# Kernel optimization log

Hardware: AMD Instinct MI355X
Metric: run time of the kernel (lower is better)

The kernel has to match this reference:

```python
import jax, jax.numpy as jnp
import numpy as np

N_HEADS = 8
N_POINTS = 4
SPATIAL = np.array([[64, 64], [32, 32], [16, 16], [8, 8]], dtype=np.int32)


def setup_inputs() -> dict:
    key = jax.random.key(0)
    ks = jax.random.split(key, 12)
    d = 256
    H, L, P, N = N_HEADS, SPATIAL.shape[0], N_POINTS, 8
    lens = SPATIAL[:, 0] * SPATIAL[:, 1]
    Lin = int(lens.sum())
    Lq = Lin
    query = jax.random.normal(ks[0], (N, Lq, d), jnp.float32)
    reference_points = jax.random.uniform(ks[1], (N, Lq, L, 2), jnp.float32)
    input_flatten = jax.random.normal(ks[2], (N, Lin, d), jnp.float32)
    input_spatial_shapes = jnp.asarray(SPATIAL)
    starts = np.concatenate([[0], np.cumsum(lens)[:-1]]).astype(np.int32)
    input_level_start_index = jnp.asarray(starts)
    s = 1.0 / np.sqrt(d)
    W_off = jax.random.normal(ks[3], (H * L * P * 2, d), jnp.float32) * 0.01
    b_off = jax.random.normal(ks[4], (H * L * P * 2,), jnp.float32) * 0.5
    W_attn = jax.random.normal(ks[5], (H * L * P, d), jnp.float32) * 0.02
    b_attn = jnp.zeros((H * L * P,), jnp.float32)
    W_val = jax.random.normal(ks[6], (d, d), jnp.float32) * s
    b_val = jnp.zeros((d,), jnp.float32)
    W_out = jax.random.normal(ks[7], (d, d), jnp.float32) * s
    b_out = jnp.zeros((d,), jnp.float32)
    return {
        'query': query, 'reference_points': reference_points,
        'input_flatten': input_flatten,
        'input_spatial_shapes': input_spatial_shapes,
        'input_level_start_index': input_level_start_index,
        'W_off': W_off, 'b_off': b_off, 'W_attn': W_attn, 'b_attn': b_attn,
        'W_val': W_val, 'b_val': b_val, 'W_out': W_out, 'b_out': b_out,
    }


def _bilinear(img, Hl, Wl, x, y):
    # img: [B, Ch, Hl*Wl]; x, y: [B, Q, P] pixel coords (align_corners=False)
    # zero padding mode: out-of-range corners contribute 0
    x0 = jnp.floor(x)
    y0 = jnp.floor(y)
    wx = x - x0
    wy = y - y0

    def gather(xi, yi):
        valid = (xi >= 0) & (xi <= Wl - 1) & (yi >= 0) & (yi <= Hl - 1)
        ii = jnp.clip(xi, 0, Wl - 1).astype(jnp.int32)
        jj = jnp.clip(yi, 0, Hl - 1).astype(jnp.int32)
        idx = jj * Wl + ii  # [B, Q, P]
        B, Q, P = idx.shape
        v = jnp.take_along_axis(img, idx.reshape(B, 1, Q * P), axis=2)
        v = v.reshape(B, img.shape[1], Q, P)
        return v * valid[:, None].astype(img.dtype)

    return (gather(x0, y0) * ((1 - wx) * (1 - wy))[:, None]
            + gather(x0 + 1, y0) * (wx * (1 - wy))[:, None]
            + gather(x0, y0 + 1) * ((1 - wx) * wy)[:, None]
            + gather(x0 + 1, y0 + 1) * (wx * wy)[:, None])


def reference(query, reference_points, input_flatten, input_spatial_shapes,
              input_level_start_index, W_off, b_off, W_attn, b_attn,
              W_val, b_val, W_out, b_out):
    shapes = np.asarray(input_spatial_shapes)  # static structural metadata
    N, Lq, d = query.shape
    Lin = input_flatten.shape[1]
    L = shapes.shape[0]
    H, P = N_HEADS, N_POINTS
    Ch = d // H

    value = input_flatten @ W_val.T + b_val                       # [N, Lin, d]
    value = value.reshape(N, Lin, H, Ch).transpose(0, 2, 3, 1)    # [N, H, Ch, Lin]
    value = value.reshape(N * H, Ch, Lin)

    off = (query @ W_off.T + b_off).reshape(N, Lq, H, L, P, 2)
    attn = (query @ W_attn.T + b_attn).reshape(N, Lq, H, L * P)
    attn = jax.nn.softmax(attn, axis=-1).reshape(N, Lq, H, L, P)

    # normalizer is (W, H) per level
    norm = jnp.asarray(np.stack([shapes[:, 1], shapes[:, 0]], -1), query.dtype)
    loc = reference_points[:, :, None, :, None, :] + off / norm[None, None, None, :, None, :]

    attn_p = attn.transpose(0, 2, 1, 3, 4).reshape(N * H, Lq, L, P)
    starts = np.concatenate([[0], np.cumsum(shapes[:, 0] * shapes[:, 1])])

    out = jnp.zeros((N * H, Ch, Lq), query.dtype)
    for l in range(L):
        Hl, Wl = int(shapes[l, 0]), int(shapes[l, 1])
        v_l = value[:, :, starts[l]:starts[l + 1]]                # [B, Ch, Hl*Wl]
        g = loc[:, :, :, l].transpose(0, 2, 1, 3, 4).reshape(N * H, Lq, P, 2)
        # grid_sample align_corners=False with grid=2*loc-1 -> pixel = loc*W - 0.5
        x = g[..., 0] * Wl - 0.5
        y = g[..., 1] * Hl - 0.5
        samp = _bilinear(v_l, Hl, Wl, x, y)                       # [B, Ch, Lq, P]
        out = out + jnp.einsum('bcqp,bqp->bcq', samp, attn_p[:, :, l])

    out = out.reshape(N, H, Ch, Lq).transpose(0, 3, 1, 2).reshape(N, Lq, d)
    return out @ W_out.T + b_out
```

## Files before the change

kernel.cpp:

```cpp
#include <hip/hip_runtime.h>
#include <hip/hip_bf16.h>

#define NQ   5440
#define NB   8
#define DIM  256
#define NH   8
#define CHN  32
#define NLV  4
#define NPT  4
#define MTOT (NB * NQ)

typedef __attribute__((ext_vector_type(8))) short s16x8;
typedef __attribute__((ext_vector_type(4))) short s16x4;
typedef __attribute__((ext_vector_type(4))) float f32x4;
typedef unsigned short ushort_t;

#define WVAL 0
#define WOFF 65536
#define WATT 131072
#define WOUT 163840
#define WTOT 229376

__device__ __forceinline__ short f2bf(float x) {
    union { __hip_bfloat16 b; short s; } u;
    u.b = __float2bfloat16(x);
    return u.s;
}

__global__ __launch_bounds__(256) void cvt_weights(const float* __restrict__ wv,
                                                   const float* __restrict__ wo,
                                                   const float* __restrict__ wa,
                                                   const float* __restrict__ wu,
                                                   ushort_t* __restrict__ wb) {
    int i = (blockIdx.x * 256 + threadIdx.x) * 4;
    if (i >= WTOT) return;
    const float* src;
    int off;
    if (i < WOFF)       { src = wv; off = WVAL; }
    else if (i < WATT)  { src = wo; off = WOFF; }
    else if (i < WOUT)  { src = wa; off = WATT; }
    else                { src = wu; off = WOUT; }
    f32x4 v = *(const f32x4*)(src + (i - off));
    s16x4 b;
#pragma unroll
    for (int e = 0; e < 4; ++e) b[e] = f2bf(v[e]);
    *(s16x4*)(wb + i) = b;
}

#define LDSK 72

__device__ __forceinline__ s16x8 load8(const float* p) {
    f32x4 a0 = *(const f32x4*)p, a1 = *(const f32x4*)(p + 4);
    s16x8 v;
#pragma unroll
    for (int e = 0; e < 4; ++e) { v[e] = f2bf(a0[e]); v[e + 4] = f2bf(a1[e]); }
    return v;
}
__device__ __forceinline__ s16x8 load8(const ushort_t* p) { return *(const s16x8*)p; }

__device__ __forceinline__ void stC(float* p, float v) { *p = v; }
__device__ __forceinline__ void stC(ushort_t* p, float v) { *(short*)p = f2bf(v); }

template <typename AT, typename CT>
__device__ __forceinline__ void gemm_core(const AT* __restrict__ A,
                                          const ushort_t* __restrict__ Wt,
                                          const float* __restrict__ biasT,
                                          CT* __restrict__ Ct, int ldC, int rowBase) {
    __shared__ short As[128 * LDSK];
    __shared__ short Ws[128 * LDSK];

    const int t = threadIdx.x;
    const int lane = t & 63, wave = t >> 6;
    const int wm = wave >> 1, wn = wave & 1;
    const int lr = lane & 15, quad = lane >> 4;

    f32x4 acc[4][4];
#pragma unroll
    for (int i = 0; i < 4; ++i)
#pragma unroll
        for (int j = 0; j < 4; ++j)
#pragma unroll
            for (int r = 0; r < 4; ++r) acc[i][j][r] = 0.f;

    for (int k0 = 0; k0 < 256; k0 += 64) {
#pragma unroll
        for (int i = 0; i < 4; ++i) {
            int c = t + i * 256;
            int r = c >> 3, kc = (c & 7) * 8;
            *(s16x8*)&As[r * LDSK + kc] = load8(A + (size_t)(rowBase + r) * DIM + k0 + kc);
            *(s16x8*)&Ws[r * LDSK + kc] = load8(Wt + (size_t)r * DIM + k0 + kc);
        }
        __syncthreads();
#pragma unroll
        for (int kk = 0; kk < 64; kk += 32) {
            s16x8 afr[4], wfr[4];
#pragma unroll
            for (int i = 0; i < 4; ++i)
                afr[i] = *(const s16x8*)&As[(wm * 64 + i * 16 + lr) * LDSK + kk + quad * 8];
#pragma unroll
            for (int j = 0; j < 4; ++j)
                wfr[j] = *(const s16x8*)&Ws[(wn * 64 + j * 16 + lr) * LDSK + kk + quad * 8];
#pragma unroll
            for (int i = 0; i < 4; ++i)
#pragma unroll
                for (int j = 0; j < 4; ++j)
                    acc[i][j] = __builtin_amdgcn_mfma_f32_16x16x32_bf16(
                        afr[i], wfr[j], acc[i][j], 0, 0, 0);
        }
        __syncthreads();
    }

    float bj[4];
#pragma unroll
    for (int j = 0; j < 4; ++j) bj[j] = biasT[wn * 64 + j * 16 + lr];
#pragma unroll
    for (int i = 0; i < 4; ++i)
#pragma unroll
        for (int r = 0; r < 4; ++r) {
            int row = rowBase + wm * 64 + i * 16 + quad * 4 + r;
#pragma unroll
            for (int j = 0; j < 4; ++j) {
                int col = wn * 64 + j * 16 + lr;
                stC(&Ct[(size_t)row * ldC + col], acc[i][j][r] + bj[j]);
            }
        }
}

__global__ __launch_bounds__(256) void gemm_val(const float* __restrict__ A,
                                                const ushort_t* __restrict__ wb,
                                                const float* __restrict__ bias,
                                                ushort_t* __restrict__ C) {
    gemm_core<float, ushort_t>(A, wb + WVAL + (size_t)blockIdx.y * 128 * DIM,
                               bias + blockIdx.y * 128, C + blockIdx.y * 128, DIM,
                               blockIdx.x * 128);
}

__global__ __launch_bounds__(256) void gemm_qkv(const float* __restrict__ A,
                                                const ushort_t* __restrict__ wb,
                                                const float* __restrict__ b_off,
                                                const float* __restrict__ b_attn,
                                                float* __restrict__ v_off,
                                                float* __restrict__ v_attn) {
    if (blockIdx.y < 2)
        gemm_core<float, float>(A, wb + WOFF + (size_t)blockIdx.y * 128 * DIM,
                                b_off + blockIdx.y * 128, v_off + blockIdx.y * 128, DIM,
                                blockIdx.x * 128);
    else
        gemm_core<float, float>(A, wb + WATT, b_attn, v_attn, 128, blockIdx.x * 128);
}

__global__ __launch_bounds__(256) void gemm_out(const ushort_t* __restrict__ A,
                                                const ushort_t* __restrict__ wb,
                                                const float* __restrict__ bias,
                                                float* __restrict__ C) {
    gemm_core<ushort_t, float>(A, wb + WOUT + (size_t)blockIdx.y * 128 * DIM,
                               bias + blockIdx.y * 128, C + blockIdx.y * 128, DIM,
                               blockIdx.x * 128);
}

__device__ __forceinline__ f32x4 bf4(uint2 u) {
    f32x4 r;
    r[0] = __uint_as_float(u.x << 16);
    r[1] = __uint_as_float(u.x & 0xffff0000u);
    r[2] = __uint_as_float(u.y << 16);
    r[3] = __uint_as_float(u.y & 0xffff0000u);
    return r;
}

__global__ __launch_bounds__(256) void sample_kernel(
    const float* __restrict__ refp,
    const float* __restrict__ off,
    const float* __restrict__ attn,
    const ushort_t* __restrict__ valb,
    const int* __restrict__ shapes,
    const int* __restrict__ starts,
    ushort_t* __restrict__ sampb)
{
    const int qBase = blockIdx.x * 4;
    const int t = threadIdx.x;

    __shared__ __align__(16) int   sidx[512][4];
    __shared__ __align__(16) float sww[512][4];

#pragma unroll
    for (int it = 0; it < 2; ++it) {
        const int i = t + it * 256;
        const int q4 = i >> 7, hlp = i & 127;
        const int h = hlp >> 4, lp = hlp & 15, l = lp >> 2, p = lp & 3;
        const int q = qBase + q4;
        const int Wl = shapes[2 * l + 1], Hl = shapes[2 * l];
        const float Wf = (float)Wl, Hf = (float)Hl;
        const float rx = refp[((size_t)q * NLV + l) * 2 + 0];
        const float ry = refp[((size_t)q * NLV + l) * 2 + 1];
        const int oidx = ((h * NLV + l) * NPT + p) * 2;
        const float ox = off[(size_t)q * DIM + oidx];
        const float oy = off[(size_t)q * DIM + oidx + 1];
        const float x = (rx + ox / Wf) * Wf - 0.5f;
        const float y = (ry + oy / Hf) * Hf - 0.5f;

        float logit = attn[(size_t)q * 128 + h * 16 + lp];
        float m = logit;
#pragma unroll
        for (int s = 8; s >= 1; s >>= 1) m = fmaxf(m, __shfl_xor(m, s, 16));
        float e = __expf(logit - m);
        float ss = e;
#pragma unroll
        for (int s = 8; s >= 1; s >>= 1) ss += __shfl_xor(ss, s, 16);
        const float aw = e / ss;

        const float xf = floorf(x), yf = floorf(y);
        const int ix = (int)xf, iy = (int)yf;
        const float wx = x - xf, wy = y - yf;
        const int ix1 = ix + 1, iy1 = iy + 1;
        const bool bx0 = (ix >= 0) & (ix < Wl);
        const bool bx1 = (ix1 >= 0) & (ix1 < Wl);
        const bool by0 = (iy >= 0) & (iy < Hl);
        const bool by1 = (iy1 >= 0) & (iy1 < Hl);
        const int cx0 = min(max(ix, 0), Wl - 1), cx1 = min(max(ix1, 0), Wl - 1);
        const int cy0 = min(max(iy, 0), Hl - 1), cy1 = min(max(iy1, 0), Hl - 1);
        const int base = starts[l];
        const int slot = (q4 << 7) + (lp << 3) + h;
        sidx[slot][0] = base + cy0 * Wl + cx0;
        sidx[slot][1] = base + cy0 * Wl + cx1;
        sidx[slot][2] = base + cy1 * Wl + cx0;
        sidx[slot][3] = base + cy1 * Wl + cx1;
        sww[slot][0] = (bx0 && by0) ? aw * (1.f - wx) * (1.f - wy) : 0.f;
        sww[slot][1] = (bx1 && by0) ? aw * wx * (1.f - wy) : 0.f;
        sww[slot][2] = (bx0 && by1) ? aw * (1.f - wx) * wy : 0.f;
        sww[slot][3] = (bx1 && by1) ? aw * wx * wy : 0.f;
    }
    __syncthreads();

    const int q4 = t >> 6, r = t & 63;
    const int h = r >> 3, c4 = (r & 7) * 4;
    const int q = qBase + q4;
    const int n = q / NQ;
    const ushort_t* vb = valb + (size_t)n * NQ * DIM + h * CHN + c4;

    f32x4 acc;
    acc[0] = acc[1] = acc[2] = acc[3] = 0.f;
#pragma unroll
    for (int lp = 0; lp < 16; ++lp) {
        const int slot = (q4 << 7) + (lp << 3) + h;
        const int4 id = *(const int4*)sidx[slot];
        const f32x4 w = *(const f32x4*)sww[slot];
        const uint2 u0 = *(const uint2*)(vb + (size_t)id.x * DIM);
        const uint2 u1 = *(const uint2*)(vb + (size_t)id.y * DIM);
        const uint2 u2 = *(const uint2*)(vb + (size_t)id.z * DIM);
        const uint2 u3 = *(const uint2*)(vb + (size_t)id.w * DIM);
        acc += bf4(u0) * w[0] + bf4(u1) * w[1] + bf4(u2) * w[2] + bf4(u3) * w[3];
    }
    s16x4 o;
#pragma unroll
    for (int e = 0; e < 4; ++e) o[e] = f2bf(acc[e]);
    *(s16x4*)(sampb + (size_t)q * DIM + h * CHN + c4) = o;
}

extern "C" void kernel_launch(void* const* d_in, const int* in_sizes, int n_in,
                              void* d_out, int out_size, void* d_ws, size_t ws_size,
                              hipStream_t stream) {
    const float* query  = (const float*)d_in[0];
    const float* refp   = (const float*)d_in[1];
    const float* inputf = (const float*)d_in[2];
    const int* shapes   = (const int*)d_in[3];
    const int* starts   = (const int*)d_in[4];
    const float* W_off  = (const float*)d_in[5];
    const float* b_off  = (const float*)d_in[6];
    const float* W_attn = (const float*)d_in[7];
    const float* b_attn = (const float*)d_in[8];
    const float* W_val  = (const float*)d_in[9];
    const float* b_val  = (const float*)d_in[10];
    const float* W_out  = (const float*)d_in[11];
    const float* b_out  = (const float*)d_in[12];
    float* out = (float*)d_out;

    char* ws = (char*)d_ws;
    ushort_t* wb     = (ushort_t*)ws;
    ushort_t* v_val  = (ushort_t*)(ws + 512 * 1024);
    float*    v_off  = (float*)(ws + 512 * 1024 + (size_t)MTOT * DIM * 2);
    float*    v_attn = (float*)((char*)v_off + (size_t)MTOT * DIM * 4);
    ushort_t* sampb  = (ushort_t*)((char*)v_attn + (size_t)MTOT * 128 * 4);

    dim3 blk(256);
    cvt_weights<<<dim3(WTOT / 1024), blk, 0, stream>>>(W_val, W_off, W_attn, W_out, wb);
    gemm_val<<<dim3(MTOT / 128, 2), blk, 0, stream>>>(inputf, wb, b_val, v_val);
    gemm_qkv<<<dim3(MTOT / 128, 3), blk, 0, stream>>>(query, wb, b_off, b_attn,
                                                      v_off, v_attn);
    sample_kernel<<<dim3(MTOT / 4), blk, 0, stream>>>(refp, v_off, v_attn, v_val,
                                                      shapes, starts, sampb);
    gemm_out<<<dim3(MTOT / 128, 2), blk, 0, stream>>>(sampb, wb, b_out, out);
}
```

Measured before the change: 292.0 us.

## Prefetch GEMM tiles into registers, merge input GEMMs, widen sampling loads

The GEMM core now loads the next K-slice of A and W into registers while the current slice is in LDS, and drops one barrier per iteration, so global latency overlaps with MFMA work. The value and offset/attention projection GEMMs are merged into one launch with a 5-wide grid. The sampling kernel handles 8 queries per block, precomputes byte offsets (including the batch base) in shared memory, and has each thread gather 8 bf16 channels with 16-byte loads instead of 4, rotating the lp order per head. This adds register pressure from the prefetch buffers, and byte offsets stored as 32-bit ints rely on the value tensor staying under 4 GB.

```diff
diff --git a/kernel.cpp b/kernel.cpp
--- a/kernel.cpp
+++ b/kernel.cpp
@@ -49,15 +49,6 @@
 
 #define LDSK 72
 
-__device__ __forceinline__ s16x8 load8(const float* p) {
-    f32x4 a0 = *(const f32x4*)p, a1 = *(const f32x4*)(p + 4);
-    s16x8 v;
-#pragma unroll
-    for (int e = 0; e < 4; ++e) { v[e] = f2bf(a0[e]); v[e + 4] = f2bf(a1[e]); }
-    return v;
-}
-__device__ __forceinline__ s16x8 load8(const ushort_t* p) { return *(const s16x8*)p; }
-
 __device__ __forceinline__ void stC(float* p, float v) { *p = v; }
 __device__ __forceinline__ void stC(ushort_t* p, float v) { *(short*)p = f2bf(v); }
 
@@ -82,13 +73,55 @@
 #pragma unroll
             for (int r = 0; r < 4; ++r) acc[i][j][r] = 0.f;
 
-    for (int k0 = 0; k0 < 256; k0 += 64) {
+    f32x4 pf0[4], pf1[4];
+    s16x8 pb[4];
+    s16x8 pw[4];
+
+#pragma unroll
+    for (int i = 0; i < 4; ++i) {
+        int c = t + i * 256, r = c >> 3, kc = (c & 7) * 8;
+        const AT* pa = A + (size_t)(rowBase + r) * DIM + kc;
+        if constexpr (sizeof(AT) == 4) {
+            pf0[i] = *(const f32x4*)pa;
+            pf1[i] = *(const f32x4*)(pa + 4);
+        } else {
+            pb[i] = *(const s16x8*)pa;
+        }
+        pw[i] = *(const s16x8*)(Wt + (size_t)r * DIM + kc);
+    }
+
+    for (int ks = 0; ks < 4; ++ks) {
+        if (ks) __syncthreads();
 #pragma unroll
         for (int i = 0; i < 4; ++i) {
-            int c = t + i * 256;
-            int r = c >> 3, kc = (c & 7) * 8;
-            *(s16x8*)&As[r * LDSK + kc] = load8(A + (size_t)(rowBase + r) * DIM + k0 + kc);
-            *(s16x8*)&Ws[r * LDSK + kc] = load8(Wt + (size_t)r * DIM + k0 + kc);
+            int c = t + i * 256, r = c >> 3, kc = (c & 7) * 8;
+            s16x8 av;
+            if constexpr (sizeof(AT) == 4) {
+#pragma unroll
+                for (int e = 0; e < 4; ++e) {
+                    av[e] = f2bf(pf0[i][e]);
+                    av[e + 4] = f2bf(pf1[i][e]);
+                }
+            } else {
+                av = pb[i];
+            }
+            *(s16x8*)&As[r * LDSK + kc] = av;
+            *(s16x8*)&Ws[r * LDSK + kc] = pw[i];
+        }
+        if (ks < 3) {
+            const int k0 = (ks + 1) * 64;
+#pragma unroll
+            for (int i = 0; i < 4; ++i) {
+                int c = t + i * 256, r = c >> 3, kc = (c & 7) * 8;
+                const AT* pa = A + (size_t)(rowBase + r) * DIM + k0 + kc;
+                if constexpr (sizeof(AT) == 4) {
+                    pf0[i] = *(const f32x4*)pa;
+                    pf1[i] = *(const f32x4*)(pa + 4);
+                } else {
+                    pb[i] = *(const s16x8*)pa;
+                }
+                pw[i] = *(const s16x8*)(Wt + (size_t)r * DIM + k0 + kc);
+            }
         }
         __syncthreads();
 #pragma unroll
@@ -107,7 +140,6 @@
                     acc[i][j] = __builtin_amdgcn_mfma_f32_16x16x32_bf16(
                         afr[i], wfr[j], acc[i][j], 0, 0, 0);
         }
-        __syncthreads();
     }
 
     float bj[4];
@@ -126,27 +158,26 @@
         }
 }
 
-__global__ __launch_bounds__(256) void gemm_val(const float* __restrict__ A,
-                                                const ushort_t* __restrict__ wb,
-                                                const float* __restrict__ bias,
-                                                ushort_t* __restrict__ C) {
-    gemm_core<float, ushort_t>(A, wb + WVAL + (size_t)blockIdx.y * 128 * DIM,
-                               bias + blockIdx.y * 128, C + blockIdx.y * 128, DIM,
-                               blockIdx.x * 128);
-}
-
-__global__ __launch_bounds__(256) void gemm_qkv(const float* __restrict__ A,
-                                                const ushort_t* __restrict__ wb,
-                                                const float* __restrict__ b_off,
-                                                const float* __restrict__ b_attn,
-                                                float* __restrict__ v_off,
-                                                float* __restrict__ v_attn) {
-    if (blockIdx.y < 2)
-        gemm_core<float, float>(A, wb + WOFF + (size_t)blockIdx.y * 128 * DIM,
-                                b_off + blockIdx.y * 128, v_off + blockIdx.y * 128, DIM,
-                                blockIdx.x * 128);
+__global__ __launch_bounds__(256) void gemm_fused(const float* __restrict__ inputf,
+                                                  const float* __restrict__ query,
+                                                  const ushort_t* __restrict__ wb,
+                                                  const float* __restrict__ b_val,
+                                                  const float* __restrict__ b_off,
+                                                  const float* __restrict__ b_attn,
+                                                  ushort_t* __restrict__ v_val,
+                                                  float* __restrict__ v_off,
+                                                  float* __restrict__ v_attn) {
+    const int gy = blockIdx.y;
+    const int rowBase = blockIdx.x * 128;
+    if (gy < 2)
+        gemm_core<float, ushort_t>(inputf, wb + WVAL + (size_t)gy * 128 * DIM,
+                                   b_val + gy * 128, v_val + gy * 128, DIM, rowBase);
+    else if (gy < 4)
+        gemm_core<float, float>(query, wb + WOFF + (size_t)(gy - 2) * 128 * DIM,
+                                b_off + (gy - 2) * 128, v_off + (gy - 2) * 128, DIM,
+                                rowBase);
     else
-        gemm_core<float, float>(A, wb + WATT, b_attn, v_attn, 128, blockIdx.x * 128);
+        gemm_core<float, float>(query, wb + WATT, b_attn, v_attn, 128, rowBase);
 }
 
 __global__ __launch_bounds__(256) void gemm_out(const ushort_t* __restrict__ A,
@@ -156,15 +187,6 @@
     gemm_core<ushort_t, float>(A, wb + WOUT + (size_t)blockIdx.y * 128 * DIM,
                                bias + blockIdx.y * 128, C + blockIdx.y * 128, DIM,
                                blockIdx.x * 128);
-}
-
-__device__ __forceinline__ f32x4 bf4(uint2 u) {
-    f32x4 r;
-    r[0] = __uint_as_float(u.x << 16);
-    r[1] = __uint_as_float(u.x & 0xffff0000u);
-    r[2] = __uint_as_float(u.y << 16);
-    r[3] = __uint_as_float(u.y & 0xffff0000u);
-    return r;
 }
 
 __global__ __launch_bounds__(256) void sample_kernel(
@@ -176,27 +198,25 @@
     const int* __restrict__ starts,
     ushort_t* __restrict__ sampb)
 {
-    const int qBase = blockIdx.x * 4;
+    const int qBase = blockIdx.x * 8;
     const int t = threadIdx.x;
 
-    __shared__ __align__(16) int   sidx[512][4];
-    __shared__ __align__(16) float sww[512][4];
-
-#pragma unroll
-    for (int it = 0; it < 2; ++it) {
+    __shared__ __align__(16) int   sidx[1024][4];
+    __shared__ __align__(16) float sww[1024][4];
+
+#pragma unroll
+    for (int it = 0; it < 4; ++it) {
         const int i = t + it * 256;
-        const int q4 = i >> 7, hlp = i & 127;
-        const int h = hlp >> 4, lp = hlp & 15, l = lp >> 2, p = lp & 3;
-        const int q = qBase + q4;
+        const int q8 = i >> 7, hlp = i & 127;
+        const int h = hlp >> 4, lp = hlp & 15, l = lp >> 2;
+        const int q = qBase + q8;
+        const int n = q / NQ;
         const int Wl = shapes[2 * l + 1], Hl = shapes[2 * l];
         const float Wf = (float)Wl, Hf = (float)Hl;
-        const float rx = refp[((size_t)q * NLV + l) * 2 + 0];
-        const float ry = refp[((size_t)q * NLV + l) * 2 + 1];
-        const int oidx = ((h * NLV + l) * NPT + p) * 2;
-        const float ox = off[(size_t)q * DIM + oidx];
-        const float oy = off[(size_t)q * DIM + oidx + 1];
-        const float x = (rx + ox / Wf) * Wf - 0.5f;
-        const float y = (ry + oy / Hf) * Hf - 0.5f;
+        const float2 rp = *(const float2*)(refp + ((size_t)q * NLV + l) * 2);
+        const float2 oo = *(const float2*)(off + (size_t)q * DIM + h * 32 + lp * 2);
+        const float x = (rp.x + oo.x / Wf) * Wf - 0.5f;
+        const float y = (rp.y + oo.y / Hf) * Hf - 0.5f;
 
         float logit = attn[(size_t)q * 128 + h * 16 + lp];
         float m = logit;
@@ -218,42 +238,67 @@
         const bool by1 = (iy1 >= 0) & (iy1 < Hl);
         const int cx0 = min(max(ix, 0), Wl - 1), cx1 = min(max(ix1, 0), Wl - 1);
         const int cy0 = min(max(iy, 0), Hl - 1), cy1 = min(max(iy1, 0), Hl - 1);
-        const int base = starts[l];
-        const int slot = (q4 << 7) + (lp << 3) + h;
-        sidx[slot][0] = base + cy0 * Wl + cx0;
-        sidx[slot][1] = base + cy0 * Wl + cx1;
-        sidx[slot][2] = base + cy1 * Wl + cx0;
-        sidx[slot][3] = base + cy1 * Wl + cx1;
-        sww[slot][0] = (bx0 && by0) ? aw * (1.f - wx) * (1.f - wy) : 0.f;
-        sww[slot][1] = (bx1 && by0) ? aw * wx * (1.f - wy) : 0.f;
-        sww[slot][2] = (bx0 && by1) ? aw * (1.f - wx) * wy : 0.f;
-        sww[slot][3] = (bx1 && by1) ? aw * wx * wy : 0.f;
+        const int base = n * NQ + starts[l];
+        int4 id;
+        id.x = (base + cy0 * Wl + cx0) << 9;
+        id.y = (base + cy0 * Wl + cx1) << 9;
+        id.z = (base + cy1 * Wl + cx0) << 9;
+        id.w = (base + cy1 * Wl + cx1) << 9;
+        f32x4 w;
+        w[0] = (bx0 && by0) ? aw * (1.f - wx) * (1.f - wy) : 0.f;
+        w[1] = (bx1 && by0) ? aw * wx * (1.f - wy) : 0.f;
+        w[2] = (bx0 && by1) ? aw * (1.f - wx) * wy : 0.f;
+        w[3] = (bx1 && by1) ? aw * wx * wy : 0.f;
+        *(int4*)sidx[i] = id;
+        *(f32x4*)sww[i] = w;
     }
     __syncthreads();
 
-    const int q4 = t >> 6, r = t & 63;
-    const int h = r >> 3, c4 = (r & 7) * 4;
-    const int q = qBase + q4;
-    const int n = q / NQ;
-    const ushort_t* vb = valb + (size_t)n * NQ * DIM + h * CHN + c4;
-
-    f32x4 acc;
-    acc[0] = acc[1] = acc[2] = acc[3] = 0.f;
-#pragma unroll
-    for (int lp = 0; lp < 16; ++lp) {
-        const int slot = (q4 << 7) + (lp << 3) + h;
+    const int q8 = t >> 5, r = t & 31;
+    const int h = r >> 2, cg = r & 3;
+    const int q = qBase + q8;
+    const char* vb = (const char*)valb + h * 64 + cg * 16;
+
+    f32x4 acc0, acc1;
+    acc0[0] = acc0[1] = acc0[2] = acc0[3] = 0.f;
+    acc1[0] = acc1[1] = acc1[2] = acc1[3] = 0.f;
+#pragma unroll
+    for (int j = 0; j < 16; ++j) {
+        const int lp = (j + h) & 15;
+        const int slot = (q8 << 7) + (h << 4) + lp;
         const int4 id = *(const int4*)sidx[slot];
         const f32x4 w = *(const f32x4*)sww[slot];
-        const uint2 u0 = *(const uint2*)(vb + (size_t)id.x * DIM);
-        const uint2 u1 = *(const uint2*)(vb + (size_t)id.y * DIM);
-        const uint2 u2 = *(const uint2*)(vb + (size_t)id.z * DIM);
-        const uint2 u3 = *(const uint2*)(vb + (size_t)id.w * DIM);
-        acc += bf4(u0) * w[0] + bf4(u1) * w[1] + bf4(u2) * w[2] + bf4(u3) * w[3];
-    }
-    s16x4 o;
-#pragma unroll
-    for (int e = 0; e < 4; ++e) o[e] = f2bf(acc[e]);
-    *(s16x4*)(sampb + (size_t)q * DIM + h * CHN + c4) = o;
+        const uint4 u0 = *(const uint4*)(vb + (size_t)(unsigned)id.x);
+        const uint4 u1 = *(const uint4*)(vb + (size_t)(unsigned)id.y);
+        const uint4 u2 = *(const uint4*)(vb + (size_t)(unsigned)id.z);
+        const uint4 u3 = *(const uint4*)(vb + (size_t)(unsigned)id.w);
+#define ACC8(u, wgt)                                                          \
+        {                                                                     \
+            f32x4 lo, hi;                                                     \
+            lo[0] = __uint_as_float(u.x << 16);                               \
+            lo[1] = __uint_as_float(u.x & 0xffff0000u);                       \
+            lo[2] = __uint_as_float(u.y << 16);                               \
+            lo[3] = __uint_as_float(u.y & 0xffff0000u);                       \
+            hi[0] = __uint_as_float(u.z << 16);                               \
+            hi[1] = __uint_as_float(u.z & 0xffff0000u);                       \
+            hi[2] = __uint_as_float(u.w << 16);                               \
+            hi[3] = __uint_as_float(u.w & 0xffff0000u);                       \
+            acc0 += lo * (wgt);                                               \
+            acc1 += hi * (wgt);                                               \
+        }
+        ACC8(u0, w[0]);
+        ACC8(u1, w[1]);
+        ACC8(u2, w[2]);
+        ACC8(u3, w[3]);
+#undef ACC8
+    }
+    s16x8 o;
+#pragma unroll
+    for (int e = 0; e < 4; ++e) {
+        o[e] = f2bf(acc0[e]);
+        o[e + 4] = f2bf(acc1[e]);
+    }
+    *(s16x8*)(sampb + (size_t)q * DIM + h * CHN + cg * 8) = o;
 }
 
 extern "C" void kernel_launch(void* const* d_in, const int* in_sizes, int n_in,
@@ -283,10 +328,10 @@
 
     dim3 blk(256);
     cvt_weights<<<dim3(WTOT / 1024), blk, 0, stream>>>(W_val, W_off, W_attn, W_out, wb);
-    gemm_val<<<dim3(MTOT / 128, 2), blk, 0, stream>>>(inputf, wb, b_val, v_val);
-    gemm_qkv<<<dim3(MTOT / 128, 3), blk, 0, stream>>>(query, wb, b_off, b_attn,
-                                                      v_off, v_attn);
-    sample_kernel<<<dim3(MTOT / 4), blk, 0, stream>>>(refp, v_off, v_attn, v_val,
+    gemm_fused<<<dim3(MTOT / 128, 5), blk, 0, stream>>>(inputf, query, wb, b_val,
+                                                        b_off, b_attn, v_val, v_off,
+                                                        v_attn);
+    sample_kernel<<<dim3(MTOT / 8), blk, 0, stream>>>(refp, v_off, v_attn, v_val,
                                                       shapes, starts, sampb);
     gemm_out<<<dim3(MTOT / 128, 2), blk, 0, stream>>>(sampb, wb, b_out, out);
 }
```

New measurement: 279.5 us. 4.3% less time.
